# Kernel tuning notes

Measured on AMD Instinct MI355X. Metric: run time of the kernel, lower is better.

Reference implementation:

```python
import jax, jax.numpy as jnp
import numpy as np

NUM_HEADS = 32
NUM_KV_HEADS = 8
HEAD_DIM = 128
SCALE = 1.0 / np.sqrt(HEAD_DIM)
BATCH = 16
MAX_CTX = 2048
NUM_SLOTS = BATCH * MAX_CTX + BATCH  # 32784; last BATCH slots are the write targets


def setup_inputs() -> dict:
    key = jax.random.key(0)
    ks = jax.random.split(key, 8)
    q = jax.random.normal(ks[0], (BATCH, NUM_HEADS, HEAD_DIM), dtype=jnp.float32)
    k = jax.random.normal(ks[1], (BATCH, NUM_KV_HEADS, HEAD_DIM), dtype=jnp.float32)
    v = jax.random.normal(ks[2], (BATCH, NUM_KV_HEADS, HEAD_DIM), dtype=jnp.float32)
    k_cache = jax.random.normal(ks[3], (NUM_SLOTS, NUM_KV_HEADS, HEAD_DIM), dtype=jnp.float32)
    v_cache = jax.random.normal(ks[4], (NUM_SLOTS, NUM_KV_HEADS, HEAD_DIM), dtype=jnp.float32)
    # each decode token writes its new kv into a fresh slot at the end of the pool
    slot_mapping = (BATCH * MAX_CTX + jnp.arange(BATCH)).astype(jnp.int64)
    # sparse-controller-selected active slots per request (paged, irregular)
    active_slots = jax.random.randint(ks[5], (BATCH, MAX_CTX), 0, NUM_SLOTS).astype(jnp.int64)
    # make the current token's slot the last active slot of its own request
    active_slots = active_slots.at[:, -1].set(slot_mapping)
    context_lens = jax.random.randint(ks[6], (BATCH,), 1, MAX_CTX + 1).astype(jnp.int64)
    return {
        "q": q, "k": k, "v": v,
        "k_cache": k_cache, "v_cache": v_cache,
        "slot_mapping": slot_mapping,
        "active_slots": active_slots,
        "context_lens": context_lens,
    }


def _attend(q, k, v, k_cache, v_cache, slot_mapping, active_slots, context_lens):
    # store_kvcache: scatter new k/v into flat slot cache; slot == -1 is skipped
    safe_slots = jnp.where(slot_mapping < 0, NUM_SLOTS, slot_mapping)  # OOB -> dropped
    kc = k_cache.at[safe_slots].set(k, mode="drop")
    vc = v_cache.at[safe_slots].set(v, mode="drop")

    # paged gather of the per-request active KV pages
    K = kc[active_slots]  # [B, L, Hkv, D]
    V = vc[active_slots]  # [B, L, Hkv, D]

    B, H, D = q.shape
    G = H // NUM_KV_HEADS  # GQA group size
    qg = q.reshape(B, NUM_KV_HEADS, G, D)

    # flash-decode stage1+stage2 == numerically-stable softmax attention over active slots
    scores = jnp.einsum("bkgd,blkd->bkgl", qg, K) * SCALE  # [B, Hkv, G, L]
    valid = jnp.arange(active_slots.shape[1])[None, :] < context_lens[:, None]  # [B, L]
    scores = jnp.where(valid[:, None, None, :], scores, jnp.float32(-1e30))
    p = jax.nn.softmax(scores, axis=-1)
    o = jnp.einsum("bkgl,blkd->bkgd", p, V).reshape(B, H, D)
    return o


def reference(q, k, v, k_cache, v_cache, slot_mapping, active_slots, context_lens):
    return _attend(q, k, v, k_cache, v_cache, slot_mapping, active_slots, context_lens)
```

## Files before the change

kernel.cpp:

```cpp
#include <hip/hip_runtime.h>
#include <hip/hip_bf16.h>
#include <float.h>

#define B 16
#define H 32
#define HKV 8
#define G 4
#define D 128
#define LMAX 2048
#define SCALE 0.08838834764831844f

template <int NSPLIT>
__global__ __launch_bounds__(256) void attn_partial(
    const float* __restrict__ q,
    const float* __restrict__ kin,
    const float* __restrict__ vin,
    const float* __restrict__ kc,
    const float* __restrict__ vc,
    const int*  __restrict__ slot_mapping,
    const int*  __restrict__ active_slots,
    const int*  __restrict__ context_lens,
    float* __restrict__ part_o,
    float* __restrict__ part_ml)
{
    constexpr int CHUNK = LMAX / NSPLIT;
    const int tid = threadIdx.x;
    int idx = blockIdx.x;
    const int split = idx % NSPLIT; idx /= NSPLIT;
    const int h = idx % HKV;
    const int b = idx / HKV;

    const int ctx   = context_lens[b];
    const int start = split * CHUNK;
    int nvalid = ctx - start;
    if (nvalid > CHUNK) nvalid = CHUNK;

    const size_t pbase = ((size_t)(b * HKV + h) * NSPLIT + split) * G;

    if (nvalid <= 0) {
        if (tid < G * 2) part_ml[pbase * 2 + tid] = (tid & 1) ? 0.f : -FLT_MAX;
        return;
    }

    __shared__ float sc[G][CHUNK];
    __shared__ const float* kp[CHUNK];
    __shared__ const float* vp[CHUNK];
    __shared__ float red[8][G][D];
    __shared__ int   sm[16];

    if (tid < 16) sm[tid] = slot_mapping[tid];
    __syncthreads();

    for (int li = tid; li < nvalid; li += 256) {
        const int s = active_slots[b * LMAX + start + li];
        int ov = -1;
#pragma unroll
        for (int j = 0; j < 16; ++j)
            if (sm[j] == s) ov = j;
        if (ov >= 0) {
            kp[li] = kin + ((size_t)ov * HKV + h) * D;
            vp[li] = vin + ((size_t)ov * HKV + h) * D;
        } else {
            kp[li] = kc + ((size_t)s * HKV + h) * D;
            vp[li] = vc + ((size_t)s * HKV + h) * D;
        }
    }
    __syncthreads();

    const int grp   = tid >> 3;
    const int lane8 = tid & 7;

    float4 qv[G][4];
#pragma unroll
    for (int g = 0; g < G; ++g) {
        const float* qp = q + ((size_t)(b * H + h * G + g)) * D;
#pragma unroll
        for (int i = 0; i < 4; ++i) {
            float4 t = *(const float4*)(qp + i * 32 + lane8 * 4);
            qv[g][i] = make_float4(t.x * SCALE, t.y * SCALE, t.z * SCALE, t.w * SCALE);
        }
    }

    for (int li = grp; li < nvalid; li += 32) {
        const float* kb = kp[li];
        float pd0 = 0.f, pd1 = 0.f, pd2 = 0.f, pd3 = 0.f;
#pragma unroll
        for (int i = 0; i < 4; ++i) {
            float4 kv = *(const float4*)(kb + i * 32 + lane8 * 4);
            pd0 += kv.x * qv[0][i].x + kv.y * qv[0][i].y + kv.z * qv[0][i].z + kv.w * qv[0][i].w;
            pd1 += kv.x * qv[1][i].x + kv.y * qv[1][i].y + kv.z * qv[1][i].z + kv.w * qv[1][i].w;
            pd2 += kv.x * qv[2][i].x + kv.y * qv[2][i].y + kv.z * qv[2][i].z + kv.w * qv[2][i].w;
            pd3 += kv.x * qv[3][i].x + kv.y * qv[3][i].y + kv.z * qv[3][i].z + kv.w * qv[3][i].w;
        }
#pragma unroll
        for (int msk = 1; msk < 8; msk <<= 1) {
            pd0 += __shfl_xor(pd0, msk, 8);
            pd1 += __shfl_xor(pd1, msk, 8);
            pd2 += __shfl_xor(pd2, msk, 8);
            pd3 += __shfl_xor(pd3, msk, 8);
        }
        if (lane8 == 0) {
            sc[0][li] = pd0; sc[1][li] = pd1; sc[2][li] = pd2; sc[3][li] = pd3;
        }
    }
    __syncthreads();

    {
        const int g    = tid >> 6;
        const int lane = tid & 63;
        float m = -FLT_MAX;
        for (int i = lane; i < nvalid; i += 64) m = fmaxf(m, sc[g][i]);
#pragma unroll
        for (int msk = 1; msk < 64; msk <<= 1) m = fmaxf(m, __shfl_xor(m, msk, 64));
        float sum = 0.f;
        for (int i = lane; i < nvalid; i += 64) {
            float p = __expf(sc[g][i] - m);
            sc[g][i] = p;
            sum += p;
        }
#pragma unroll
        for (int msk = 1; msk < 64; msk <<= 1) sum += __shfl_xor(sum, msk, 64);
        if (lane == 0) {
            part_ml[(pbase + g) * 2 + 0] = m;
            part_ml[(pbase + g) * 2 + 1] = sum;
        }
    }
    __syncthreads();

    {
        const int grp8  = tid >> 5;
        const int dlane = tid & 31;
        const int db    = dlane * 4;
        float4 a0 = {0,0,0,0}, a1 = {0,0,0,0}, a2 = {0,0,0,0}, a3 = {0,0,0,0};
#pragma unroll 4
        for (int i = grp8; i < nvalid; i += 8) {
            const float4 vv = *(const float4*)(vp[i] + db);
            const float p0 = sc[0][i], p1 = sc[1][i], p2 = sc[2][i], p3 = sc[3][i];
            a0.x += p0 * vv.x; a0.y += p0 * vv.y; a0.z += p0 * vv.z; a0.w += p0 * vv.w;
            a1.x += p1 * vv.x; a1.y += p1 * vv.y; a1.z += p1 * vv.z; a1.w += p1 * vv.w;
            a2.x += p2 * vv.x; a2.y += p2 * vv.y; a2.z += p2 * vv.z; a2.w += p2 * vv.w;
            a3.x += p3 * vv.x; a3.y += p3 * vv.y; a3.z += p3 * vv.z; a3.w += p3 * vv.w;
        }
        *(float4*)(&red[grp8][0][db]) = a0;
        *(float4*)(&red[grp8][1][db]) = a1;
        *(float4*)(&red[grp8][2][db]) = a2;
        *(float4*)(&red[grp8][3][db]) = a3;
    }
    __syncthreads();

    {
#pragma unroll
        for (int k2 = 0; k2 < 2; ++k2) {
            const int oidx = tid * 2 + k2;
            const int g = oidx >> 7;
            const int d = oidx & 127;
            float s = 0.f;
#pragma unroll
            for (int r = 0; r < 8; ++r) s += red[r][g][d];
            part_o[(pbase + g) * D + d] = s;
        }
    }
}

__global__ __launch_bounds__(128) void attn_reduce(
    const float* __restrict__ part_o,
    const float* __restrict__ part_ml,
    float* __restrict__ out,
    int nsplit)
{
    int idx = blockIdx.x;
    const int g = idx & 3;
    const int h = (idx >> 2) & 7;
    const int b = idx >> 5;
    const int d = threadIdx.x;

    const size_t base = (size_t)(b * HKV + h) * nsplit;

    float M = -FLT_MAX;
    for (int s = 0; s < nsplit; ++s) {
        const float l = part_ml[((base + s) * G + g) * 2 + 1];
        if (l > 0.f) M = fmaxf(M, part_ml[((base + s) * G + g) * 2 + 0]);
    }
    float L = 0.f, acc = 0.f;
    for (int s = 0; s < nsplit; ++s) {
        const float l = part_ml[((base + s) * G + g) * 2 + 1];
        if (l > 0.f) {
            const float e = __expf(part_ml[((base + s) * G + g) * 2 + 0] - M);
            L += l * e;
            acc += e * part_o[((base + s) * G + g) * D + d];
        }
    }
    out[((size_t)(b * H) + h * G + g) * D + d] = acc / (L > 0.f ? L : 1.f);
}

extern "C" void kernel_launch(void* const* d_in, const int* in_sizes, int n_in,
                              void* d_out, int out_size, void* d_ws, size_t ws_size,
                              hipStream_t stream) {
    const float* q  = (const float*)d_in[0];
    const float* k  = (const float*)d_in[1];
    const float* v  = (const float*)d_in[2];
    const float* kc = (const float*)d_in[3];
    const float* vc = (const float*)d_in[4];
    const int* slot_mapping = (const int*)d_in[5];
    const int* active_slots = (const int*)d_in[6];
    const int* context_lens = (const int*)d_in[7];
    float* out = (float*)d_out;

    const size_t perSplit = (size_t)B * HKV * (G * D + G * 2) * sizeof(float);
    int nsplit = 8;
    if (ws_size >= 32 * perSplit)      nsplit = 32;
    else if (ws_size >= 16 * perSplit) nsplit = 16;

    float* part_o  = (float*)d_ws;
    float* part_ml = part_o + (size_t)B * HKV * nsplit * G * D;

    if (nsplit == 32) {
        attn_partial<32><<<B * HKV * 32, 256, 0, stream>>>(
            q, k, v, kc, vc, slot_mapping, active_slots, context_lens, part_o, part_ml);
    } else if (nsplit == 16) {
        attn_partial<16><<<B * HKV * 16, 256, 0, stream>>>(
            q, k, v, kc, vc, slot_mapping, active_slots, context_lens, part_o, part_ml);
    } else {
        attn_partial<8><<<B * HKV * 8, 256, 0, stream>>>(
            q, k, v, kc, vc, slot_mapping, active_slots, context_lens, part_o, part_ml);
    }
    attn_reduce<<<B * HKV * G, 128, 0, stream>>>(part_o, part_ml, out, nsplit);
}
```

Before: 49.50 us.

## Double-buffer gathered K/V rows into LDS via async global-to-LDS loads

Gathered K and V rows are now copied into a double-buffered LDS staging area with global_load_lds, in batches of 32 rows. The aim is to overlap the next batch's loads with the current batch's QK or PV compute. Scores are stored row-major so the PV loop can read them as one float4, and the staging buffer is reused for the final cross-group reduction. The split count drops from 32 to at most 16. The reduce kernel now caches the per-split max and sum values in LDS. In exchange, each block uses about 36 KB of LDS, which lowers occupancy, and there is a barrier per batch. Correctness also depends on the async LDS loads being complete at each barrier.

```diff
diff --git a/kernel.cpp b/kernel.cpp
--- a/kernel.cpp
+++ b/kernel.cpp
@@ -8,9 +8,20 @@
 #define G 4
 #define D 128
 #define LMAX 2048
+#define BATCH 32
 #define SCALE 0.08838834764831844f
 
-template <int NSPLIT>
+__device__ __forceinline__ void stage16(const float* gsrc, float* lds_base, int lane) {
+#if __has_builtin(__builtin_amdgcn_global_load_lds)
+    __builtin_amdgcn_global_load_lds(
+        (const __attribute__((address_space(1))) void*)gsrc,
+        (__attribute__((address_space(3))) void*)lds_base, 16, 0, 0);
+#else
+    *(float4*)((char*)lds_base + lane * 16) = *(const float4*)gsrc;
+#endif
+}
+
+template <int CHUNK>
 __global__ __launch_bounds__(256) void attn_partial(
     const float* __restrict__ q,
     const float* __restrict__ kin,
@@ -23,12 +34,11 @@
     float* __restrict__ part_o,
     float* __restrict__ part_ml)
 {
-    constexpr int CHUNK = LMAX / NSPLIT;
-    const int tid = threadIdx.x;
-    int idx = blockIdx.x;
-    const int split = idx % NSPLIT; idx /= NSPLIT;
-    const int h = idx % HKV;
-    const int b = idx / HKV;
+    constexpr int NSPLIT = LMAX / CHUNK;
+    const int tid   = threadIdx.x;
+    const int split = blockIdx.x % NSPLIT;
+    const int h     = (blockIdx.x / NSPLIT) % HKV;
+    const int b     = blockIdx.x / (NSPLIT * HKV);
 
     const int ctx   = context_lens[b];
     const int start = split * CHUNK;
@@ -42,11 +52,11 @@
         return;
     }
 
-    __shared__ float sc[G][CHUNK];
+    __shared__ float stg[2][BATCH * D];
+    __shared__ float sc[CHUNK][G];
     __shared__ const float* kp[CHUNK];
     __shared__ const float* vp[CHUNK];
-    __shared__ float red[8][G][D];
-    __shared__ int   sm[16];
+    __shared__ int sm[16];
 
     if (tid < 16) sm[tid] = slot_mapping[tid];
     __syncthreads();
@@ -57,18 +67,14 @@
 #pragma unroll
         for (int j = 0; j < 16; ++j)
             if (sm[j] == s) ov = j;
-        if (ov >= 0) {
-            kp[li] = kin + ((size_t)ov * HKV + h) * D;
-            vp[li] = vin + ((size_t)ov * HKV + h) * D;
-        } else {
-            kp[li] = kc + ((size_t)s * HKV + h) * D;
-            vp[li] = vc + ((size_t)s * HKV + h) * D;
-        }
-    }
-    __syncthreads();
+        kp[li] = (ov >= 0) ? kin + ((size_t)ov * HKV + h) * D : kc + ((size_t)s * HKV + h) * D;
+        vp[li] = (ov >= 0) ? vin + ((size_t)ov * HKV + h) * D : vc + ((size_t)s * HKV + h) * D;
+    }
 
     const int grp   = tid >> 3;
     const int lane8 = tid & 7;
+    const int wv    = tid >> 6;
+    const int lane  = tid & 63;
 
     float4 qv[G][4];
 #pragma unroll
@@ -80,42 +86,64 @@
             qv[g][i] = make_float4(t.x * SCALE, t.y * SCALE, t.z * SCALE, t.w * SCALE);
         }
     }
-
-    for (int li = grp; li < nvalid; li += 32) {
-        const float* kb = kp[li];
-        float pd0 = 0.f, pd1 = 0.f, pd2 = 0.f, pd3 = 0.f;
-#pragma unroll
-        for (int i = 0; i < 4; ++i) {
-            float4 kv = *(const float4*)(kb + i * 32 + lane8 * 4);
-            pd0 += kv.x * qv[0][i].x + kv.y * qv[0][i].y + kv.z * qv[0][i].z + kv.w * qv[0][i].w;
-            pd1 += kv.x * qv[1][i].x + kv.y * qv[1][i].y + kv.z * qv[1][i].z + kv.w * qv[1][i].w;
-            pd2 += kv.x * qv[2][i].x + kv.y * qv[2][i].y + kv.z * qv[2][i].z + kv.w * qv[2][i].w;
-            pd3 += kv.x * qv[3][i].x + kv.y * qv[3][i].y + kv.z * qv[3][i].z + kv.w * qv[3][i].w;
-        }
-#pragma unroll
-        for (int msk = 1; msk < 8; msk <<= 1) {
-            pd0 += __shfl_xor(pd0, msk, 8);
-            pd1 += __shfl_xor(pd1, msk, 8);
-            pd2 += __shfl_xor(pd2, msk, 8);
-            pd3 += __shfl_xor(pd3, msk, 8);
-        }
-        if (lane8 == 0) {
-            sc[0][li] = pd0; sc[1][li] = pd1; sc[2][li] = pd2; sc[3][li] = pd3;
-        }
-    }
-    __syncthreads();
+    __syncthreads();
+
+    const int nb = (nvalid + BATCH - 1) / BATCH;
+
+    auto STAGE = [&](const float* const* ptrs, int t, int buf) {
+#pragma unroll
+        for (int p = 0; p < 4; ++p) {
+            const int r  = wv * 8 + 2 * p + (lane >> 5);
+            const int li = t * BATCH + r;
+            if (li < nvalid)
+                stage16(ptrs[li] + (lane & 31) * 4, &stg[buf][(wv * 8 + 2 * p) * D], lane);
+        }
+    };
+
+    auto COMPUTE_QK = [&](int t, int buf) {
+        const int li = t * BATCH + grp;
+        if (li < nvalid) {
+            const float* kr = &stg[buf][grp * D];
+            float pd0 = 0.f, pd1 = 0.f, pd2 = 0.f, pd3 = 0.f;
+#pragma unroll
+            for (int j = 0; j < 4; ++j) {
+                const float4 kv = *(const float4*)(kr + j * 32 + lane8 * 4);
+                pd0 += kv.x * qv[0][j].x + kv.y * qv[0][j].y + kv.z * qv[0][j].z + kv.w * qv[0][j].w;
+                pd1 += kv.x * qv[1][j].x + kv.y * qv[1][j].y + kv.z * qv[1][j].z + kv.w * qv[1][j].w;
+                pd2 += kv.x * qv[2][j].x + kv.y * qv[2][j].y + kv.z * qv[2][j].z + kv.w * qv[2][j].w;
+                pd3 += kv.x * qv[3][j].x + kv.y * qv[3][j].y + kv.z * qv[3][j].z + kv.w * qv[3][j].w;
+            }
+#pragma unroll
+            for (int msk = 1; msk < 8; msk <<= 1) {
+                pd0 += __shfl_xor(pd0, msk, 8);
+                pd1 += __shfl_xor(pd1, msk, 8);
+                pd2 += __shfl_xor(pd2, msk, 8);
+                pd3 += __shfl_xor(pd3, msk, 8);
+            }
+            if (lane8 == 0)
+                *(float4*)&sc[li][0] = make_float4(pd0, pd1, pd2, pd3);
+        }
+    };
+
+    STAGE(kp, 0, 0);
+    __syncthreads();
+    for (int t = 0; t < nb; ++t) {
+        if (t + 1 < nb) STAGE(kp, t + 1, (t + 1) & 1);
+        else            STAGE(vp, 0, nb & 1);
+        COMPUTE_QK(t, t & 1);
+        __syncthreads();
+    }
 
     {
-        const int g    = tid >> 6;
-        const int lane = tid & 63;
+        const int g = wv;
         float m = -FLT_MAX;
-        for (int i = lane; i < nvalid; i += 64) m = fmaxf(m, sc[g][i]);
+        for (int i = lane; i < nvalid; i += 64) m = fmaxf(m, sc[i][g]);
 #pragma unroll
         for (int msk = 1; msk < 64; msk <<= 1) m = fmaxf(m, __shfl_xor(m, msk, 64));
         float sum = 0.f;
         for (int i = lane; i < nvalid; i += 64) {
-            float p = __expf(sc[g][i] - m);
-            sc[g][i] = p;
+            const float p = __expf(sc[i][g] - m);
+            sc[i][g] = p;
             sum += p;
         }
 #pragma unroll
@@ -127,36 +155,42 @@
     }
     __syncthreads();
 
+    const int grp8 = tid >> 5;
+    const int dl   = tid & 31;
+    float4 a0 = {0,0,0,0}, a1 = {0,0,0,0}, a2 = {0,0,0,0}, a3 = {0,0,0,0};
+    for (int t = 0; t < nb; ++t) {
+        if (t + 1 < nb) STAGE(vp, t + 1, (nb + t + 1) & 1);
+        const int buf = (nb + t) & 1;
+#pragma unroll
+        for (int ii = 0; ii < 4; ++ii) {
+            const int r  = ii * 8 + grp8;
+            const int li = t * BATCH + r;
+            if (li < nvalid) {
+                const float4 vv = *(const float4*)(&stg[buf][r * D + dl * 4]);
+                const float4 p4 = *(const float4*)&sc[li][0];
+                a0.x += p4.x * vv.x; a0.y += p4.x * vv.y; a0.z += p4.x * vv.z; a0.w += p4.x * vv.w;
+                a1.x += p4.y * vv.x; a1.y += p4.y * vv.y; a1.z += p4.y * vv.z; a1.w += p4.y * vv.w;
+                a2.x += p4.z * vv.x; a2.y += p4.z * vv.y; a2.z += p4.z * vv.z; a2.w += p4.z * vv.w;
+                a3.x += p4.w * vv.x; a3.y += p4.w * vv.y; a3.z += p4.w * vv.z; a3.w += p4.w * vv.w;
+            }
+        }
+        __syncthreads();
+    }
+
     {
-        const int grp8  = tid >> 5;
-        const int dlane = tid & 31;
-        const int db    = dlane * 4;
-        float4 a0 = {0,0,0,0}, a1 = {0,0,0,0}, a2 = {0,0,0,0}, a3 = {0,0,0,0};
-#pragma unroll 4
-        for (int i = grp8; i < nvalid; i += 8) {
-            const float4 vv = *(const float4*)(vp[i] + db);
-            const float p0 = sc[0][i], p1 = sc[1][i], p2 = sc[2][i], p3 = sc[3][i];
-            a0.x += p0 * vv.x; a0.y += p0 * vv.y; a0.z += p0 * vv.z; a0.w += p0 * vv.w;
-            a1.x += p1 * vv.x; a1.y += p1 * vv.y; a1.z += p1 * vv.z; a1.w += p1 * vv.w;
-            a2.x += p2 * vv.x; a2.y += p2 * vv.y; a2.z += p2 * vv.z; a2.w += p2 * vv.w;
-            a3.x += p3 * vv.x; a3.y += p3 * vv.y; a3.z += p3 * vv.z; a3.w += p3 * vv.w;
-        }
-        *(float4*)(&red[grp8][0][db]) = a0;
-        *(float4*)(&red[grp8][1][db]) = a1;
-        *(float4*)(&red[grp8][2][db]) = a2;
-        *(float4*)(&red[grp8][3][db]) = a3;
-    }
-    __syncthreads();
-
-    {
+        float* red = &stg[0][0];
+        *(float4*)&red[((grp8 * G + 0) * D) + dl * 4] = a0;
+        *(float4*)&red[((grp8 * G + 1) * D) + dl * 4] = a1;
+        *(float4*)&red[((grp8 * G + 2) * D) + dl * 4] = a2;
+        *(float4*)&red[((grp8 * G + 3) * D) + dl * 4] = a3;
+        __syncthreads();
 #pragma unroll
         for (int k2 = 0; k2 < 2; ++k2) {
-            const int oidx = tid * 2 + k2;
-            const int g = oidx >> 7;
-            const int d = oidx & 127;
+            const int o = tid * 2 + k2;
+            const int g = o >> 7, d = o & 127;
             float s = 0.f;
 #pragma unroll
-            for (int r = 0; r < 8; ++r) s += red[r][g][d];
+            for (int r = 0; r < 8; ++r) s += red[(r * G + g) * D + d];
             part_o[(pbase + g) * D + d] = s;
         }
     }
@@ -168,24 +202,29 @@
     float* __restrict__ out,
     int nsplit)
 {
-    int idx = blockIdx.x;
-    const int g = idx & 3;
-    const int h = (idx >> 2) & 7;
-    const int b = idx >> 5;
+    const int g = blockIdx.x & 3;
+    const int h = (blockIdx.x >> 2) & 7;
+    const int b = blockIdx.x >> 5;
     const int d = threadIdx.x;
 
+    __shared__ float mlds[32], llds[32];
     const size_t base = (size_t)(b * HKV + h) * nsplit;
 
+    for (int s = d; s < nsplit; s += 128) {
+        mlds[s] = part_ml[((base + s) * G + g) * 2 + 0];
+        llds[s] = part_ml[((base + s) * G + g) * 2 + 1];
+    }
+    __syncthreads();
+
     float M = -FLT_MAX;
-    for (int s = 0; s < nsplit; ++s) {
-        const float l = part_ml[((base + s) * G + g) * 2 + 1];
-        if (l > 0.f) M = fmaxf(M, part_ml[((base + s) * G + g) * 2 + 0]);
-    }
+    for (int s = 0; s < nsplit; ++s)
+        if (llds[s] > 0.f) M = fmaxf(M, mlds[s]);
+
     float L = 0.f, acc = 0.f;
     for (int s = 0; s < nsplit; ++s) {
-        const float l = part_ml[((base + s) * G + g) * 2 + 1];
+        const float l = llds[s];
         if (l > 0.f) {
-            const float e = __expf(part_ml[((base + s) * G + g) * 2 + 0] - M);
+            const float e = __expf(mlds[s] - M);
             L += l * e;
             acc += e * part_o[((base + s) * G + g) * D + d];
         }
@@ -207,21 +246,16 @@
     float* out = (float*)d_out;
 
     const size_t perSplit = (size_t)B * HKV * (G * D + G * 2) * sizeof(float);
-    int nsplit = 8;
-    if (ws_size >= 32 * perSplit)      nsplit = 32;
-    else if (ws_size >= 16 * perSplit) nsplit = 16;
+    const int nsplit = (ws_size >= 16 * perSplit) ? 16 : 8;
 
     float* part_o  = (float*)d_ws;
     float* part_ml = part_o + (size_t)B * HKV * nsplit * G * D;
 
-    if (nsplit == 32) {
-        attn_partial<32><<<B * HKV * 32, 256, 0, stream>>>(
-            q, k, v, kc, vc, slot_mapping, active_slots, context_lens, part_o, part_ml);
-    } else if (nsplit == 16) {
-        attn_partial<16><<<B * HKV * 16, 256, 0, stream>>>(
+    if (nsplit == 16) {
+        attn_partial<128><<<B * HKV * 16, 256, 0, stream>>>(
             q, k, v, kc, vc, slot_mapping, active_slots, context_lens, part_o, part_ml);
     } else {
-        attn_partial<8><<<B * HKV * 8, 256, 0, stream>>>(
+        attn_partial<256><<<B * HKV * 8, 256, 0, stream>>>(
             q, k, v, kc, vc, slot_mapping, active_slots, context_lens, part_o, part_ml);
     }
     attn_reduce<<<B * HKV * G, 128, 0, stream>>>(part_o, part_ml, out, nsplit);
```

After: 43.01 us. 1.15x faster.
